# Optimization experiments

Measured on AMD Instinct MI355X. Metric: run time of the kernel, lower is better.

## Reference

```python
import jax, jax.numpy as jnp
import numpy as np
from jax.scipy.special import logsumexp

K = 64
N = 1048576
NS = 1024


def setup_inputs() -> dict:
    key = jax.random.key(0)
    k1, k2, k3 = jax.random.split(key, 3)
    return {
        "log_pdf": jax.random.normal(k1, (K, N), dtype=jnp.float32),
        "pi": jax.random.normal(k2, (K,), dtype=jnp.float32),
        "T": jax.random.normal(k3, (K, K), dtype=jnp.float32),
        "samples_per_sequence": NS,
    }


def reference(log_pdf, pi, T, samples_per_sequence):
    # log_pdf: (K, N); pi: (K,); T: (K, K); samples_per_sequence: python int Ns
    Kdim, Ndim = log_pdf.shape
    Ns = int(samples_per_sequence)
    B = Ndim // Ns  # number of equal-length sequences
    log_T = jax.nn.log_softmax(T, axis=1)   # LogSoftmax_T(dim=1)
    log_pi = jax.nn.log_softmax(pi, axis=0)  # LogSoftmax_pi(dim=0)
    # torch: log_pdf.T.view(B, Ns, K) -> time-major (Ns, B, K)
    lp_time = log_pdf.T.reshape(B, Ns, Kdim).transpose(1, 0, 2)
    alpha0 = lp_time[0] + log_pi[None, :]  # (B, K)

    def step(alpha, lp_t):
        # logsumexp over previous state j: alpha[b, j] + log_T[j, k]
        new = lp_t + logsumexp(alpha[:, :, None] + log_T[None, :, :], axis=1)
        return new, None

    alpha_last, _ = jax.lax.scan(step, alpha0, lp_time[1:])
    return jnp.sum(logsumexp(alpha_last, axis=-1))
```

## Files before the change

kernel.cpp:

```cpp
#include <hip/hip_runtime.h>

#define KSTATE 64
#define NSAMP  1024

__device__ __forceinline__ float bcast0(float x) {
  return __int_as_float(__builtin_amdgcn_readfirstlane(__float_as_int(x)));
}
__device__ __forceinline__ float rlane(float x, int l) {
  return __int_as_float(__builtin_amdgcn_readlane(__float_as_int(x), l));
}

__global__ __launch_bounds__(64) void hmm_preproc(
    const float* __restrict__ pi, const float* __restrict__ T,
    float* __restrict__ expT, float* __restrict__ log_pi,
    float* __restrict__ out) {
  const int lane = threadIdx.x;
  float m = -3.4e38f;
  for (int k = 0; k < KSTATE; ++k) m = fmaxf(m, T[lane * KSTATE + k]);
  float s = 0.f;
  for (int k = 0; k < KSTATE; ++k) s += __expf(T[lane * KSTATE + k] - m);
  float inv = 1.0f / s;
  for (int k = 0; k < KSTATE; ++k)
    expT[lane * KSTATE + k] = __expf(T[lane * KSTATE + k] - m) * inv;
  float x = pi[lane];
  float mm = x;
  #pragma unroll
  for (int off = 32; off >= 1; off >>= 1) mm = fmaxf(mm, __shfl_xor(mm, off, 64));
  float e = __expf(x - mm);
  #pragma unroll
  for (int off = 32; off >= 1; off >>= 1) e += __shfl_xor(e, off, 64);
  log_pi[lane] = x - mm - __logf(e);
  if (lane == 0) out[0] = 0.f;
}

__global__ __launch_bounds__(256) void hmm_forward(
    const float* __restrict__ log_pdf,
    const float* __restrict__ expT,
    const float* __restrict__ log_pi,
    float* __restrict__ out, int N) {
  const int lane = threadIdx.x & 63;
  const int wave = threadIdx.x >> 6;
  const int b = blockIdx.x * 4 + wave;

  float tcol[KSTATE];
  #pragma unroll
  for (int j = 0; j < KSTATE; ++j) tcol[j] = expT[j * KSTATE + lane];

  const float* lp = log_pdf + (size_t)lane * (size_t)N + (size_t)b * NSAMP;

  float4 v0 = *(const float4*)(lp);
  float4 r1 = *(const float4*)(lp + 4);
  float4 r2 = *(const float4*)(lp + 8);

  float x0 = v0.x + log_pi[lane];
  float C = bcast0(x0);
  float a = __expf(x0 - C);

#define STEP(ELP) do {                                                        \
    float s0 = 0.f, s1 = 0.f, s2 = 0.f, s3 = 0.f;                             \
    _Pragma("unroll")                                                         \
    for (int j = 0; j < KSTATE; j += 4) {                                     \
      float p0 = rlane(a, j + 0);                                             \
      float p1 = rlane(a, j + 1);                                             \
      float p2 = rlane(a, j + 2);                                             \
      float p3 = rlane(a, j + 3);                                             \
      s0 = fmaf(p0, tcol[j + 0], s0);                                         \
      s1 = fmaf(p1, tcol[j + 1], s1);                                         \
      s2 = fmaf(p2, tcol[j + 2], s2);                                         \
      s3 = fmaf(p3, tcol[j + 3], s3);                                         \
    }                                                                         \
    a = ((s0 + s1) + (s2 + s3)) * (ELP);                                      \
  } while (0)

#define RENORM() do {                                                         \
    float c = bcast0(a);                                                      \
    a = a * __builtin_amdgcn_rcpf(c);                                         \
    C += __logf(c);                                                           \
  } while (0)

  {
    float e1 = __expf(v0.y), e2 = __expf(v0.z), e3 = __expf(v0.w);
    STEP(e1); STEP(e2); STEP(e3);
    RENORM();
  }

  const int NG = NSAMP / 4;
  for (int g = 1; g < NG; ++g) {
    float4 v = r1; r1 = r2;
    int gn = (g + 2 < NG) ? (g + 2) : (NG - 1);
    r2 = *(const float4*)(lp + 4 * gn);
    float e0 = __expf(v.x), e1 = __expf(v.y), e2 = __expf(v.z), e3 = __expf(v.w);
    STEP(e0); STEP(e1); STEP(e2); STEP(e3);
    RENORM();
  }
#undef STEP
#undef RENORM

  float s = a;
  #pragma unroll
  for (int off = 32; off >= 1; off >>= 1) s += __shfl_xor(s, off, 64);
  if (lane == 0) atomicAdd(out, C + __logf(s));
}

extern "C" void kernel_launch(void* const* d_in, const int* in_sizes, int n_in,
                              void* d_out, int out_size, void* d_ws, size_t ws_size,
                              hipStream_t stream) {
  const float* log_pdf = (const float*)d_in[0];
  const float* pi      = (const float*)d_in[1];
  const float* T       = (const float*)d_in[2];
  float* out = (float*)d_out;

  float* expT   = (float*)d_ws;
  float* log_pi = expT + KSTATE * KSTATE;

  const int N = in_sizes[0] / KSTATE;
  const int B = N / NSAMP;

  hipLaunchKernelGGL(hmm_preproc, dim3(1), dim3(64), 0, stream,
                     pi, T, expT, log_pi, out);
  hipLaunchKernelGGL(hmm_forward, dim3(B / 4), dim3(256), 0, stream,
                     log_pdf, expT, log_pi, out, N);
}
```

Before: 533.2 us.

## Split each sequence's state reduction across two waves with LDS exchange

```diff
diff --git a/kernel.cpp b/kernel.cpp
--- a/kernel.cpp
+++ b/kernel.cpp
@@ -33,43 +33,51 @@
   if (lane == 0) out[0] = 0.f;
 }
 
-__global__ __launch_bounds__(256) void hmm_forward(
+__global__ __launch_bounds__(128) void hmm_forward(
     const float* __restrict__ log_pdf,
     const float* __restrict__ expT,
     const float* __restrict__ log_pi,
     float* __restrict__ out, int N) {
+  __shared__ __align__(8) float pbuf[2][2][KSTATE];
   const int lane = threadIdx.x & 63;
-  const int wave = threadIdx.x >> 6;
-  const int b = blockIdx.x * 4 + wave;
+  const int h  = __builtin_amdgcn_readfirstlane(threadIdx.x >> 6);
+  const int oh = 1 - h;
+  const int jbase = h * 32;
+  const int b = blockIdx.x;
 
-  float tcol[KSTATE];
+  float tcol[32];
   #pragma unroll
-  for (int j = 0; j < KSTATE; ++j) tcol[j] = expT[j * KSTATE + lane];
+  for (int jj = 0; jj < 32; ++jj) tcol[jj] = expT[(jbase + jj) * KSTATE + lane];
 
   const float* lp = log_pdf + (size_t)lane * (size_t)N + (size_t)b * NSAMP;
 
   float4 v0 = *(const float4*)(lp);
   float4 r1 = *(const float4*)(lp + 4);
   float4 r2 = *(const float4*)(lp + 8);
+  float4 r3 = *(const float4*)(lp + 12);
 
   float x0 = v0.x + log_pi[lane];
   float C = bcast0(x0);
   float a = __expf(x0 - C);
 
-#define STEP(ELP) do {                                                        \
+#define STEP(E, PAR) do {                                                     \
     float s0 = 0.f, s1 = 0.f, s2 = 0.f, s3 = 0.f;                             \
     _Pragma("unroll")                                                         \
-    for (int j = 0; j < KSTATE; j += 4) {                                     \
-      float p0 = rlane(a, j + 0);                                             \
-      float p1 = rlane(a, j + 1);                                             \
-      float p2 = rlane(a, j + 2);                                             \
-      float p3 = rlane(a, j + 3);                                             \
-      s0 = fmaf(p0, tcol[j + 0], s0);                                         \
-      s1 = fmaf(p1, tcol[j + 1], s1);                                         \
-      s2 = fmaf(p2, tcol[j + 2], s2);                                         \
-      s3 = fmaf(p3, tcol[j + 3], s3);                                         \
+    for (int jj = 0; jj < 32; jj += 4) {                                      \
+      float p0 = rlane(a, jbase + jj + 0);                                    \
+      float p1 = rlane(a, jbase + jj + 1);                                    \
+      float p2 = rlane(a, jbase + jj + 2);                                    \
+      float p3 = rlane(a, jbase + jj + 3);                                    \
+      s0 = fmaf(p0, tcol[jj + 0], s0);                                        \
+      s1 = fmaf(p1, tcol[jj + 1], s1);                                        \
+      s2 = fmaf(p2, tcol[jj + 2], s2);                                        \
+      s3 = fmaf(p3, tcol[jj + 3], s3);                                        \
     }                                                                         \
-    a = ((s0 + s1) + (s2 + s3)) * (ELP);                                      \
+    float part = (s0 + s1) + (s2 + s3);                                       \
+    pbuf[PAR][h][lane] = part;                                                \
+    __syncthreads();                                                          \
+    float oth = pbuf[PAR][oh][lane];                                          \
+    a = (part + oth) * (E);                                                   \
   } while (0)
 
 #define RENORM() do {                                                         \
@@ -80,17 +88,17 @@
 
   {
     float e1 = __expf(v0.y), e2 = __expf(v0.z), e3 = __expf(v0.w);
-    STEP(e1); STEP(e2); STEP(e3);
+    STEP(e1, 0); STEP(e2, 1); STEP(e3, 0);
     RENORM();
   }
 
   const int NG = NSAMP / 4;
   for (int g = 1; g < NG; ++g) {
-    float4 v = r1; r1 = r2;
-    int gn = (g + 2 < NG) ? (g + 2) : (NG - 1);
-    r2 = *(const float4*)(lp + 4 * gn);
+    float4 v = r1; r1 = r2; r2 = r3;
+    int gn = (g + 3 < NG) ? (g + 3) : (NG - 1);
+    r3 = *(const float4*)(lp + 4 * gn);
     float e0 = __expf(v.x), e1 = __expf(v.y), e2 = __expf(v.z), e3 = __expf(v.w);
-    STEP(e0); STEP(e1); STEP(e2); STEP(e3);
+    STEP(e0, 1); STEP(e1, 0); STEP(e2, 1); STEP(e3, 0);
     RENORM();
   }
 #undef STEP
@@ -99,7 +107,7 @@
   float s = a;
   #pragma unroll
   for (int off = 32; off >= 1; off >>= 1) s += __shfl_xor(s, off, 64);
-  if (lane == 0) atomicAdd(out, C + __logf(s));
+  if (threadIdx.x == 0) atomicAdd(out, C + __logf(s));
 }
 
 extern "C" void kernel_launch(void* const* d_in, const int* in_sizes, int n_in,
@@ -118,6 +126,6 @@
 
   hipLaunchKernelGGL(hmm_preproc, dim3(1), dim3(64), 0, stream,
                      pi, T, expT, log_pi, out);
-  hipLaunchKernelGGL(hmm_forward, dim3(B / 4), dim3(256), 0, stream,
+  hipLaunchKernelGGL(hmm_forward, dim3(B), dim3(128), 0, stream,
                      log_pdf, expT, log_pi, out, N);
 }
```

Result: slower. 842.2 us (+57.9%).

## Broadcast alpha via LDS plus DPP quad-perm FMAC instead of per-lane readlane

Applied to the files above, without the earlier changes.

```diff
diff --git a/kernel.cpp b/kernel.cpp
--- a/kernel.cpp
+++ b/kernel.cpp
@@ -33,14 +33,33 @@
   if (lane == 0) out[0] = 0.f;
 }
 
+#define FMACQ(ACC, SRC, TC, Q)                                                \
+  __asm__ volatile("v_fmac_f32_dpp %0, %1, %2 quad_perm:[" #Q "," #Q "," #Q   \
+                   "," #Q "] row_mask:0xf bank_mask:0xf"                      \
+                   : "+v"(ACC) : "v"(SRC), "v"(TC))
+
+#define DPPQ(Q) do {                                                          \
+    FMACQ(c0, A0.x, tcol[16*Q+ 0], Q); FMACQ(c1, A0.y, tcol[16*Q+ 1], Q);     \
+    FMACQ(c2, A0.z, tcol[16*Q+ 2], Q); FMACQ(c3, A0.w, tcol[16*Q+ 3], Q);     \
+    FMACQ(c4, A1.x, tcol[16*Q+ 4], Q); FMACQ(c5, A1.y, tcol[16*Q+ 5], Q);     \
+    FMACQ(c6, A1.z, tcol[16*Q+ 6], Q); FMACQ(c7, A1.w, tcol[16*Q+ 7], Q);     \
+    FMACQ(c0, A2.x, tcol[16*Q+ 8], Q); FMACQ(c1, A2.y, tcol[16*Q+ 9], Q);     \
+    FMACQ(c2, A2.z, tcol[16*Q+10], Q); FMACQ(c3, A2.w, tcol[16*Q+11], Q);     \
+    FMACQ(c4, A3.x, tcol[16*Q+12], Q); FMACQ(c5, A3.y, tcol[16*Q+13], Q);     \
+    FMACQ(c6, A3.z, tcol[16*Q+14], Q); FMACQ(c7, A3.w, tcol[16*Q+15], Q);     \
+  } while (0)
+
 __global__ __launch_bounds__(256) void hmm_forward(
     const float* __restrict__ log_pdf,
     const float* __restrict__ expT,
     const float* __restrict__ log_pi,
     float* __restrict__ out, int N) {
+  __shared__ __align__(16) float abuf[4][KSTATE];
   const int lane = threadIdx.x & 63;
   const int wave = threadIdx.x >> 6;
   const int b = blockIdx.x * 4 + wave;
+  float* ab = abuf[wave];
+  const float* myread = ab + 16 * (lane & 3);
 
   float tcol[KSTATE];
   #pragma unroll
@@ -51,25 +70,36 @@
   float4 v0 = *(const float4*)(lp);
   float4 r1 = *(const float4*)(lp + 4);
   float4 r2 = *(const float4*)(lp + 8);
+  float4 r3 = *(const float4*)(lp + 12);
 
   float x0 = v0.x + log_pi[lane];
   float C = bcast0(x0);
   float a = __expf(x0 - C);
 
-#define STEP(ELP) do {                                                        \
-    float s0 = 0.f, s1 = 0.f, s2 = 0.f, s3 = 0.f;                             \
-    _Pragma("unroll")                                                         \
-    for (int j = 0; j < KSTATE; j += 4) {                                     \
-      float p0 = rlane(a, j + 0);                                             \
-      float p1 = rlane(a, j + 1);                                             \
-      float p2 = rlane(a, j + 2);                                             \
-      float p3 = rlane(a, j + 3);                                             \
-      s0 = fmaf(p0, tcol[j + 0], s0);                                         \
-      s1 = fmaf(p1, tcol[j + 1], s1);                                         \
-      s2 = fmaf(p2, tcol[j + 2], s2);                                         \
-      s3 = fmaf(p3, tcol[j + 3], s3);                                         \
-    }                                                                         \
-    a = ((s0 + s1) + (s2 + s3)) * (ELP);                                      \
+#define STEP(E) do {                                                          \
+    ab[lane] = a;                                           \
+    float4 A0 = *(const float4*)(myread + 0);          \
+    float4 A1 = *(const float4*)(myread + 4);                                 \
+    float4 A2 = *(const float4*)(myread + 8);                                 \
+    float4 A3 = *(const float4*)(myread + 12);                                \
+            \
+    float c0 = rlane(a, 0) * tcol[0],  c1 = rlane(a, 1) * tcol[1];            \
+    float c2 = rlane(a, 2) * tcol[2],  c3 = rlane(a, 3) * tcol[3];            \
+    float c4 = rlane(a, 4) * tcol[4],  c5 = rlane(a, 5) * tcol[5];            \
+    float c6 = rlane(a, 6) * tcol[6],  c7 = rlane(a, 7) * tcol[7];            \
+    c0 = fmaf(rlane(a,  8), tcol[ 8], c0);                                    \
+    c1 = fmaf(rlane(a,  9), tcol[ 9], c1);                                    \
+    c2 = fmaf(rlane(a, 10), tcol[10], c2);                                    \
+    c3 = fmaf(rlane(a, 11), tcol[11], c3);                                    \
+    c4 = fmaf(rlane(a, 12), tcol[12], c4);                                    \
+    c5 = fmaf(rlane(a, 13), tcol[13], c5);                                    \
+    c6 = fmaf(rlane(a, 14), tcol[14], c6);                                    \
+    c7 = fmaf(rlane(a, 15), tcol[15], c7);                                    \
+    __asm__ volatile("s_waitcnt lgkmcnt(0)" ::: "memory");                    \
+    DPPQ(1); DPPQ(2); DPPQ(3);                   \
+    float sA = (c0 + c1) + (c2 + c3);                                         \
+    float sB = (c4 + c5) + (c6 + c7);                                         \
+    a = (sA + sB) * (E);                                                      \
   } while (0)
 
 #define RENORM() do {                                                         \
@@ -86,9 +116,9 @@
 
   const int NG = NSAMP / 4;
   for (int g = 1; g < NG; ++g) {
-    float4 v = r1; r1 = r2;
-    int gn = (g + 2 < NG) ? (g + 2) : (NG - 1);
-    r2 = *(const float4*)(lp + 4 * gn);
+    float4 v = r1; r1 = r2; r2 = r3;
+    int gn = (g + 3 < NG) ? (g + 3) : (NG - 1);
+    r3 = *(const float4*)(lp + 4 * gn);
     float e0 = __expf(v.x), e1 = __expf(v.y), e2 = __expf(v.z), e3 = __expf(v.w);
     STEP(e0); STEP(e1); STEP(e2); STEP(e3);
     RENORM();
```

Result: faster. 513.2 us (-3.8%).
